# Kernel optimization log

Measured on AMD Instinct MI355X. Metric: run time of the kernel, lower is better.

## Reference

```python
import jax, jax.numpy as jnp
import numpy as np
from jax import lax

V, E, H = 32000, 512, 512
B, T = 16, 128


def setup_inputs() -> dict:
    key = jax.random.key(0)
    ks = jax.random.split(key, 10)
    xs = jax.random.randint(ks[0], (B, T), 0, V)
    xs_len = jax.random.randint(ks[1], (B,), 1, T)
    enc_h = jax.random.normal(ks[2], (1, B, H), dtype=jnp.float32)
    enc_c = jax.random.normal(ks[3], (1, B, H), dtype=jnp.float32)
    emb = jax.random.normal(ks[4], (V, E), dtype=jnp.float32) * 0.02
    emb = emb.at[0].set(0.0)  # padding_idx=0
    s = 1.0 / np.sqrt(H)
    W_ih = jax.random.uniform(ks[5], (4 * H, E), minval=-s, maxval=s, dtype=jnp.float32)
    W_hh = jax.random.uniform(ks[6], (4 * H, H), minval=-s, maxval=s, dtype=jnp.float32)
    b_ih = jax.random.uniform(ks[7], (4 * H,), minval=-s, maxval=s, dtype=jnp.float32)
    b_hh = jax.random.uniform(ks[8], (4 * H,), minval=-s, maxval=s, dtype=jnp.float32)
    W_out = jax.random.normal(ks[9], (V, H), dtype=jnp.float32) * 0.02
    b_out = jnp.zeros((V,), dtype=jnp.float32)
    return {"xs": xs, "xs_len": xs_len, "enc_h": enc_h, "enc_c": enc_c,
            "emb": emb, "W_ih": W_ih, "W_hh": W_hh, "b_ih": b_ih,
            "b_hh": b_hh, "W_out": W_out, "b_out": b_out}


def reference(xs, xs_len, enc_h, enc_c, emb, W_ih, W_hh, b_ih, b_hh, W_out, b_out):
    exs = emb[xs]                         # [B, T, E]
    exs_t = jnp.transpose(exs, (1, 0, 2))  # time-major [T, B, E]

    def step(carry, x):
        h, c = carry
        gates = x @ W_ih.T + b_ih + h @ W_hh.T + b_hh  # [B, 4H]
        i, f, g, o = jnp.split(gates, 4, axis=-1)
        i = jax.nn.sigmoid(i)
        f = jax.nn.sigmoid(f)
        g = jnp.tanh(g)
        o = jax.nn.sigmoid(o)
        c = f * c + i * g
        h = o * jnp.tanh(c)
        return (h, c), h

    _, hs = lax.scan(step, (enc_h[0], enc_c[0]), exs_t)  # hs: [T, B, H]
    cat_hs = hs.reshape(T * B, H)          # torch.cat(hs_list, dim=0)
    logits = cat_hs @ W_out.T + b_out      # [T*B, V]
    return logits
```

## Files before the change

### kernel.cpp

```cpp
#include <hip/hip_runtime.h>
#include <stdint.h>
#include <stddef.h>

#define AS1 __attribute__((address_space(1)))
#define AS3 __attribute__((address_space(3)))

typedef __attribute__((ext_vector_type(4))) float f32x4;
typedef __attribute__((ext_vector_type(8))) short bf16x8;

static __device__ __forceinline__ unsigned short f2b(float x) {
  union { float f; uint32_t u; } c; c.f = x;
  return (unsigned short)((c.u + 0x7FFFu + ((c.u >> 16) & 1u)) >> 16);
}
static __device__ __forceinline__ float fsig(float x) {
  return __builtin_amdgcn_rcpf(1.f + __expf(-x));
}
static __device__ __forceinline__ float ftanh(float x) {
  return 1.f - 2.f * __builtin_amdgcn_rcpf(__expf(2.f * x) + 1.f);
}

#define AGLD(p) __hip_atomic_load((p), __ATOMIC_RELAXED, __HIP_MEMORY_SCOPE_AGENT)
#define AGST(p, v) __hip_atomic_store((p), (v), __ATOMIC_RELAXED, __HIP_MEMORY_SCOPE_AGENT)


__global__ __launch_bounds__(128) void k_cvt_perm(const float* __restrict__ s,
                                                  unsigned short* __restrict__ d) {
  int rp = blockIdx.x;
  int w = rp >> 6, q = (rp >> 4) & 3, j = rp & 15;
  int rs = q * 512 + w * 16 + j;
  float4 v = ((const float4*)(s + (size_t)rs * 512))[threadIdx.x];
  ushort4 o;
  o.x = f2b(v.x); o.y = f2b(v.y); o.z = f2b(v.z); o.w = f2b(v.w);
  ((ushort4*)(d + (size_t)rp * 512))[threadIdx.x] = o;
}

__global__ __launch_bounds__(256) void k_bias_perm(const float* __restrict__ a,
                                                   const float* __restrict__ b,
                                                   float* __restrict__ o) {
  int rp = blockIdx.x * 256 + threadIdx.x;
  if (rp < 2048) {
    int w = rp >> 6, q = (rp >> 4) & 3, j = rp & 15;
    int rs = q * 512 + w * 16 + j;
    o[rp] = a[rs] + b[rs];
  }
}

__global__ __launch_bounds__(128) void k_emb_gather(const int* __restrict__ xs,
                                                    const float* __restrict__ emb,
                                                    unsigned short* __restrict__ out) {
  int m = blockIdx.x;
  int tok = xs[(m & 15) * 128 + (m >> 4)];
  float4 v = ((const float4*)(emb + (size_t)tok * 512))[threadIdx.x];
  ushort4 o;
  o.x = f2b(v.x); o.y = f2b(v.y); o.z = f2b(v.z); o.w = f2b(v.w);
  ((ushort4*)(out + (size_t)m * 512))[threadIdx.x] = o;
}

__global__ __launch_bounds__(256) void k_ench(const float* __restrict__ ench,
                                              unsigned short* __restrict__ hsb) {
  int idx = blockIdx.x * 256 + threadIdx.x;
  int b = idx >> 9, c = idx & 511;
  hsb[(c >> 4) * 256 + b * 16 + (c & 15)] = f2b(ench[b * 512 + c]);
}

__global__ __launch_bounds__(256) void k_gemm_bt(const unsigned short* __restrict__ A,
                                                 const unsigned short* __restrict__ Bt,
                                                 const float* __restrict__ bias,
                                                 float* __restrict__ C,
                                                 int M, int N, int K) {
  __shared__ unsigned short As[128 * 32];
  __shared__ unsigned short Bs[128 * 32];
  const int tiles_n = N >> 7;
  const int tm = blockIdx.x / tiles_n;
  const int tn = blockIdx.x % tiles_n;
  const int m0 = tm << 7, n0 = tn << 7;
  const int tid = threadIdx.x;
  const int wave = tid >> 6, lane = tid & 63;
  const int wr = wave >> 1, wc = wave & 1;
  f32x4 acc[4][4] = {};

  const int lo = wave * 2048 + lane * 16;
  for (int k0 = 0; k0 < K; k0 += 32) {
#pragma unroll
    for (int i = 0; i < 2; ++i) {
      int o = lo + i * 1024;
      int row = o >> 6, kb = o & 63;
      __builtin_amdgcn_global_load_lds(
          (const AS1 uint32_t*)((const char*)A + ((size_t)(m0 + row) * K + k0) * 2 + kb),
          (AS3 uint32_t*)((char*)As + wave * 2048 + i * 1024), 16, 0, 0);
    }
#pragma unroll
    for (int i = 0; i < 2; ++i) {
      int o = lo + i * 1024;
      int row = o >> 6, kb = o & 63;
      __builtin_amdgcn_global_load_lds(
          (const AS1 uint32_t*)((const char*)Bt + ((size_t)(n0 + row) * K + k0) * 2 + kb),
          (AS3 uint32_t*)((char*)Bs + wave * 2048 + i * 1024), 16, 0, 0);
    }
    __syncthreads();
    bf16x8 af[4], bfr[4];
    const int lrow = lane & 15;
    const int kb16 = (lane >> 4) * 16;
#pragma unroll
    for (int i = 0; i < 4; ++i)
      af[i] = *(const bf16x8*)((const char*)As + (wr * 64 + i * 16 + lrow) * 64 + kb16);
#pragma unroll
    for (int j = 0; j < 4; ++j)
      bfr[j] = *(const bf16x8*)((const char*)Bs + (wc * 64 + j * 16 + lrow) * 64 + kb16);
#pragma unroll
    for (int i = 0; i < 4; ++i)
#pragma unroll
      for (int j = 0; j < 4; ++j)
        acc[i][j] = __builtin_amdgcn_mfma_f32_16x16x32_bf16(af[i], bfr[j], acc[i][j], 0, 0, 0);
    __syncthreads();
  }
#pragma unroll
  for (int j = 0; j < 4; ++j) {
    int col = n0 + wc * 64 + j * 16 + (lane & 15);
    float bv = bias[col];
#pragma unroll
    for (int i = 0; i < 4; ++i) {
      int r0 = m0 + wr * 64 + i * 16 + (lane >> 4) * 4;
#pragma unroll
      for (int r = 0; r < 4; ++r)
        C[(size_t)(r0 + r) * N + col] = acc[i][j][r] + bv;
    }
  }
}


__global__ __launch_bounds__(256, 1) void k_fused(
    const float* __restrict__ gp, const unsigned short* __restrict__ wp,
    const float* __restrict__ encc, unsigned short* __restrict__ hsb,
    uint32_t* __restrict__ flags, uint32_t* __restrict__ progress,
    const float* __restrict__ Wout, unsigned short* __restrict__ woutb,
    const float* __restrict__ bout, float* __restrict__ out,
    uint32_t* __restrict__ ticket, uint32_t* __restrict__ cvt_done) {
  __shared__ unsigned short Bs[128 * 32];
  __shared__ int sh_tile;
  __shared__ int sh_rdy;

  const int bid = blockIdx.x;
  const int tid = threadIdx.x;

  const uint64_t K1 = 0x0001000100010001ull;
  const uint64_t K8 = 0x8000800080008000ull;

  if (bid < 32) {
    if (tid >= 64) return;
    const int w = bid;
    const int l = tid;
    const int lr = l & 15;
    const int lk = l >> 4;
    const int col = w * 16 + lr;

    bf16x8 bfr[4][16];
#pragma unroll
    for (int j = 0; j < 4; ++j)
#pragma unroll
      for (int ks = 0; ks < 16; ++ks)
        bfr[j][ks] = *(const bf16x8*)((const char*)wp +
            (size_t)(w * 64 + j * 16 + lr) * 1024 + ks * 64 + lk * 16);

    float cst[4];
#pragma unroll
    for (int r = 0; r < 4; ++r) cst[r] = encc[(lk * 4 + r) * 512 + col];

    const int u64off = (lk >> 1) * 64 + lr * 4 + (lk & 1) * 2;

    float gnx[4][4];
#pragma unroll
    for (int j = 0; j < 4; ++j)
#pragma unroll
      for (int r = 0; r < 4; ++r)
        gnx[j][r] = gp[(size_t)(lk * 4 + r) * 2048 + w * 64 + j * 16 + lr];

    for (int t = 0; t < 128; ++t) {
      f32x4 acc[4];
#pragma unroll
      for (int j = 0; j < 4; ++j)
#pragma unroll
        for (int r = 0; r < 4; ++r) acc[j][r] = gnx[j][r];

      union AF { uint64_t q[2]; bf16x8 v; } af[16];
      const uint64_t* hb = (const uint64_t*)(hsb + (size_t)t * 8192);
      {
        int guard = 0;
        for (;;) {
#pragma unroll
          for (int ks = 0; ks < 16; ++ks) {
            af[ks].q[0] = AGLD(hb + u64off + ks * 128);
            af[ks].q[1] = AGLD(hb + u64off + ks * 128 + 1);
          }
          uint64_t bad = 0;
#pragma unroll
          for (int ks = 0; ks < 16; ++ks) {
            bad |= (~af[ks].q[0] - K1) & af[ks].q[0] & K8;
            bad |= (~af[ks].q[1] - K1) & af[ks].q[1] & K8;
          }
          if (__all(bad == 0)) break;
          if (++guard > (1 << 20)) break;
        }
      }

#pragma unroll
      for (int ks = 0; ks < 16; ++ks) {
#pragma unroll
        for (int j = 0; j < 4; ++j)
          acc[j] = __builtin_amdgcn_mfma_f32_16x16x32_bf16(af[ks].v, bfr[j][ks],
                                                           acc[j], 0, 0, 0);
      }

      uint32_t pk[4];
#pragma unroll
      for (int r = 0; r < 4; ++r) {
        float iv = fsig(acc[0][r]);
        float fv = fsig(acc[1][r]);
        float gv = ftanh(acc[2][r]);
        float ov = fsig(acc[3][r]);
        cst[r] = fv * cst[r] + iv * gv;
        float hv = ov * ftanh(cst[r]);
        uint32_t mine = f2b(hv);
        uint32_t other = (uint32_t)__shfl_xor((int)mine, 1);
        pk[r] = mine | (other << 16);
      }
      uint32_t* hout = (uint32_t*)(hsb + (size_t)(t + 1) * 8192);
      if ((lr & 1) == 0) {
#pragma unroll
        for (int r = 0; r < 4; ++r)
          AGST(hout + w * 128 + (lk * 4 + r) * 8 + (lr >> 1), pk[r]);
      }
      if ((t & 7) == 7 && l == 0)
        AGST(flags + (size_t)(t >> 3) * 32 + w, 1u);

      if (t < 127) {
#pragma unroll
        for (int j = 0; j < 4; ++j)
#pragma unroll
          for (int r = 0; r < 4; ++r)
            gnx[j][r] = gp[(size_t)((t + 1) * 16 + lk * 4 + r) * 2048 +
                           w * 64 + j * 16 + lr];
      }
    }
  } else if (bid == 32) {
    if (tid >= 64) return;
    const int l = tid;
    for (int g = 0; g < 16; ++g) {
      int guard = 0;
      for (;;) {
        uint32_t fl = AGLD(flags + (size_t)g * 32 + (l & 31));
        if (__all(fl != 0u)) break;
        __builtin_amdgcn_s_sleep(4);
        if (++guard > (1 << 18)) break;
      }
      if (l < 8)
        AGST(progress + l * 64, (uint32_t)((g + 1) * 8));
    }
  } else {
    {
      const int gid = bid - 33;
      const int CH = 19052;
      int start = gid * CH;
      int end = start + CH; if (end > 4096000) end = 4096000;
      for (int idx = start + tid; idx < end; idx += 256) {
        float4 v = ((const float4*)Wout)[idx];
        uint32_t lo2 = (uint32_t)f2b(v.x) | ((uint32_t)f2b(v.y) << 16);
        uint32_t hi2 = (uint32_t)f2b(v.z) | ((uint32_t)f2b(v.w) << 16);
        AGST((uint64_t*)woutb + idx, (uint64_t)lo2 | ((uint64_t)hi2 << 32));
      }
      asm volatile("s_waitcnt vmcnt(0)" ::: "memory");
      __syncthreads();
      if (tid == 0) {
        atomicAdd(cvt_done, 1u);
        sh_rdy = 0;
      }
      __syncthreads();
      int guard = 0;
      for (;;) {
        if (tid == 0 && AGLD(cvt_done) >= 215u) sh_rdy = 1;
        __syncthreads();
        if (sh_rdy) break;
        __builtin_amdgcn_s_sleep(16);
        if (++guard > (1 << 18)) break;
        __syncthreads();
      }
    }

    const int wave = tid >> 6, lane = tid & 63;
    const int wr = wave >> 1, wc = wave & 1;
    const int lrow = lane & 15;
    const int ksl = lane >> 4;
    const int lo = wave * 2048 + lane * 16;
    const uint32_t* prog = progress + (bid & 7) * 64;
    const uint64_t* Ab64 = (const uint64_t*)(hsb + 8192);

    for (;;) {
      if (tid == 0) sh_tile = (int)atomicAdd(ticket, 1u);
      __syncthreads();
      const int tk = sh_tile;
      __syncthreads();
      if (tk >= 730) break;
      int m, nb0, ntiles;
      if (tk < 480) {
        m = tk >> 5;
        nb0 = (tk & 31) * 8;
        ntiles = (250 - nb0) < 8 ? (250 - nb0) : 8;
      } else {
        m = 15;
        nb0 = tk - 480;
        ntiles = 1;
      }
      const int m0 = m << 7;
      const uint32_t need = (uint32_t)(m * 8 + 8);

      if (tid == 0) sh_rdy = 0;
      __syncthreads();
      {
        int guard = 0;
        for (;;) {
          if (tid == 0) {
            uint32_t v = AGLD(prog);
            if (v >= need) sh_rdy = 1;
          }
          __syncthreads();
          if (sh_rdy) break;
          __builtin_amdgcn_s_sleep(48);
          if (++guard > (1 << 16)) break;
          __syncthreads();
        }
      }

      {
        int ph = tk & 7;
        for (int s = 0; s < ph; ++s) __builtin_amdgcn_s_sleep(16);
      }

      bf16x8 Areg[16][4];
      {
        int guard = 0;
        for (;;) {
          uint64_t bad = 0;
#pragma unroll
          for (int ks = 0; ks < 16; ++ks)
#pragma unroll
            for (int i = 0; i < 4; ++i) {
              const uint64_t* ap = Ab64 + (size_t)(m * 8 + wr * 4 + i) * 2048 +
                  (2 * ks + (ksl >> 1)) * 64 + lrow * 4 + (ksl & 1) * 2;
              union { uint64_t q[2]; bf16x8 v; } u;
              u.q[0] = AGLD(ap);
              u.q[1] = AGLD(ap + 1);
              bad |= ((~u.q[0] - K1) & u.q[0] & K8) |
                     ((~u.q[1] - K1) & u.q[1] & K8);
              Areg[ks][i] = u.v;
            }
          if (__all(bad == 0)) break;
          __builtin_amdgcn_s_sleep(4);
          if (++guard > (1 << 20)) break;
        }
      }

      for (int jt = 0; jt < ntiles; ++jt) {
        const int n0 = (nb0 + jt) << 7;
        f32x4 acc[4][4] = {};
#pragma unroll
        for (int ks = 0; ks < 16; ++ks) {
#pragma unroll
          for (int i = 0; i < 2; ++i) {
            int o = lo + i * 1024;
            int row = o >> 6, kb = o & 63;
            __builtin_amdgcn_global_load_lds(
                (const AS1 uint32_t*)((const char*)woutb +
                    ((size_t)(n0 + row) * 512 + ks * 32) * 2 + kb),
                (AS3 uint32_t*)((char*)Bs + o), 16, 0, 0);
          }
          __syncthreads();
          bf16x8 bfr[4];
#pragma unroll
          for (int j = 0; j < 4; ++j)
            bfr[j] = *(const bf16x8*)((const char*)Bs +
                (wc * 64 + j * 16 + lrow) * 64 + ksl * 16);
#pragma unroll
          for (int i = 0; i < 4; ++i)
#pragma unroll
            for (int j = 0; j < 4; ++j)
              acc[i][j] = __builtin_amdgcn_mfma_f32_16x16x32_bf16(
                  Areg[ks][i], bfr[j], acc[i][j], 0, 0, 0);
          __syncthreads();
        }
#pragma unroll
        for (int j = 0; j < 4; ++j) {
          int colq = n0 + wc * 64 + j * 16 + (lane & 15);
          float bv = bout[colq];
#pragma unroll
          for (int i = 0; i < 4; ++i) {
            int r0 = m0 + wr * 64 + i * 16 + (lane >> 4) * 4;
#pragma unroll
            for (int r = 0; r < 4; ++r)
              out[(size_t)(r0 + r) * 32000 + colq] = acc[i][j][r] + bv;
          }
        }
      }
    }
  }
}


extern "C" void kernel_launch(void* const* d_in, const int* in_sizes, int n_in,
                              void* d_out, int out_size, void* d_ws, size_t ws_size,
                              hipStream_t stream) {
  (void)in_sizes; (void)n_in; (void)out_size; (void)ws_size;
  const int* xs = (const int*)d_in[0];
  const float* ench = (const float*)d_in[2];
  const float* encc = (const float*)d_in[3];
  const float* emb  = (const float*)d_in[4];
  const float* Wih  = (const float*)d_in[5];
  const float* Whh  = (const float*)d_in[6];
  const float* bih  = (const float*)d_in[7];
  const float* bhh  = (const float*)d_in[8];
  const float* Wout = (const float*)d_in[9];
  const float* bout = (const float*)d_in[10];
  float* out = (float*)d_out;

  char* ws = (char*)d_ws;
  size_t off = 0;
  auto take = [&](size_t bytes) {
    char* p = ws + off;
    off += (bytes + 255) & ~(size_t)255;
    return p;
  };
  float* gates_pre      = (float*)take(2048ull * 2048 * 4);
  unsigned short* hsb   = (unsigned short*)take(129ull * 16 * 512 * 2);
  unsigned short* aemb  = (unsigned short*)take(2048ull * 512 * 2);
  unsigned short* wih_b = (unsigned short*)take(2048ull * 512 * 2);
  unsigned short* wp_b  = (unsigned short*)take(2048ull * 512 * 2);
  unsigned short* wout_b= (unsigned short*)take(32000ull * 512 * 2);
  float* bias1          = (float*)take(2048 * 4);
  uint32_t* flags       = (uint32_t*)take(16ull * 32 * 4);
  uint32_t* progress    = (uint32_t*)take(8 * 256);
  uint32_t* ticket      = (uint32_t*)take(256);
  uint32_t* cvt_done    = (uint32_t*)take(256);

  k_cvt_perm<<<2048, 128, 0, stream>>>(Wih, wih_b);
  k_cvt_perm<<<2048, 128, 0, stream>>>(Whh, wp_b);
  k_emb_gather<<<2048, 128, 0, stream>>>(xs, emb, aemb);
  k_bias_perm<<<8, 256, 0, stream>>>(bih, bhh, bias1);

  k_ench<<<32, 256, 0, stream>>>(ench, hsb);
  hipMemsetAsync(hsb + 16 * 512, 0xFF, 128ull * 16 * 512 * 2, stream);
  hipMemsetAsync(flags, 0, 16ull * 32 * 4, stream);
  hipMemsetAsync(progress, 0, 8 * 256, stream);
  hipMemsetAsync(ticket, 0, 256, stream);
  hipMemsetAsync(cvt_done, 0, 256, stream);

  k_gemm_bt<<<256, 256, 0, stream>>>(aemb, wih_b, bias1, gates_pre, 2048, 2048, 512);

  k_fused<<<248, 256, 0, stream>>>(gates_pre, wp_b, encc, hsb, flags, progress,
                                   Wout, wout_b, bout, out, ticket, cvt_done);
}
```

Before: 425.8 us.

## Fuse input-projection GEMM into persistent kernel, overlapping with recurrence via sentinels

Removes the separate input-gate GEMM launch and has the worker blocks of the persistent kernel compute the gates_pre tiles through a ticket counter. The recurrent blocks poll gates_pre for a 0xFF sentinel, which is set by a memset, before consuming each timestep, so the recurrence can start before the GEMM finishes. Progress flags are also made per-timestep instead of every 8 steps, so the output GEMM can follow the recurrence more closely. The cost is an extra 16MB memset, spin polling on gates_pre, and a wait (waitcnt) before each flag store.

```diff
diff --git a/kernel.cpp b/kernel.cpp
--- a/kernel.cpp
+++ b/kernel.cpp
@@ -63,71 +63,6 @@
   hsb[(c >> 4) * 256 + b * 16 + (c & 15)] = f2b(ench[b * 512 + c]);
 }
 
-__global__ __launch_bounds__(256) void k_gemm_bt(const unsigned short* __restrict__ A,
-                                                 const unsigned short* __restrict__ Bt,
-                                                 const float* __restrict__ bias,
-                                                 float* __restrict__ C,
-                                                 int M, int N, int K) {
-  __shared__ unsigned short As[128 * 32];
-  __shared__ unsigned short Bs[128 * 32];
-  const int tiles_n = N >> 7;
-  const int tm = blockIdx.x / tiles_n;
-  const int tn = blockIdx.x % tiles_n;
-  const int m0 = tm << 7, n0 = tn << 7;
-  const int tid = threadIdx.x;
-  const int wave = tid >> 6, lane = tid & 63;
-  const int wr = wave >> 1, wc = wave & 1;
-  f32x4 acc[4][4] = {};
-
-  const int lo = wave * 2048 + lane * 16;
-  for (int k0 = 0; k0 < K; k0 += 32) {
-#pragma unroll
-    for (int i = 0; i < 2; ++i) {
-      int o = lo + i * 1024;
-      int row = o >> 6, kb = o & 63;
-      __builtin_amdgcn_global_load_lds(
-          (const AS1 uint32_t*)((const char*)A + ((size_t)(m0 + row) * K + k0) * 2 + kb),
-          (AS3 uint32_t*)((char*)As + wave * 2048 + i * 1024), 16, 0, 0);
-    }
-#pragma unroll
-    for (int i = 0; i < 2; ++i) {
-      int o = lo + i * 1024;
-      int row = o >> 6, kb = o & 63;
-      __builtin_amdgcn_global_load_lds(
-          (const AS1 uint32_t*)((const char*)Bt + ((size_t)(n0 + row) * K + k0) * 2 + kb),
-          (AS3 uint32_t*)((char*)Bs + wave * 2048 + i * 1024), 16, 0, 0);
-    }
-    __syncthreads();
-    bf16x8 af[4], bfr[4];
-    const int lrow = lane & 15;
-    const int kb16 = (lane >> 4) * 16;
-#pragma unroll
-    for (int i = 0; i < 4; ++i)
-      af[i] = *(const bf16x8*)((const char*)As + (wr * 64 + i * 16 + lrow) * 64 + kb16);
-#pragma unroll
-    for (int j = 0; j < 4; ++j)
-      bfr[j] = *(const bf16x8*)((const char*)Bs + (wc * 64 + j * 16 + lrow) * 64 + kb16);
-#pragma unroll
-    for (int i = 0; i < 4; ++i)
-#pragma unroll
-      for (int j = 0; j < 4; ++j)
-        acc[i][j] = __builtin_amdgcn_mfma_f32_16x16x32_bf16(af[i], bfr[j], acc[i][j], 0, 0, 0);
-    __syncthreads();
-  }
-#pragma unroll
-  for (int j = 0; j < 4; ++j) {
-    int col = n0 + wc * 64 + j * 16 + (lane & 15);
-    float bv = bias[col];
-#pragma unroll
-    for (int i = 0; i < 4; ++i) {
-      int r0 = m0 + wr * 64 + i * 16 + (lane >> 4) * 4;
-#pragma unroll
-      for (int r = 0; r < 4; ++r)
-        C[(size_t)(r0 + r) * N + col] = acc[i][j][r] + bv;
-    }
-  }
-}
-
 
 __global__ __launch_bounds__(256, 1) void k_fused(
     const float* __restrict__ gp, const unsigned short* __restrict__ wp,
@@ -135,7 +70,11 @@
     uint32_t* __restrict__ flags, uint32_t* __restrict__ progress,
     const float* __restrict__ Wout, unsigned short* __restrict__ woutb,
     const float* __restrict__ bout, float* __restrict__ out,
-    uint32_t* __restrict__ ticket, uint32_t* __restrict__ cvt_done) {
+    const unsigned short* __restrict__ aemb, const unsigned short* __restrict__ wihb,
+    const float* __restrict__ bias1, float* __restrict__ gates_pre,
+    uint32_t* __restrict__ ticket, uint32_t* __restrict__ ticket_g,
+    uint32_t* __restrict__ cvt_done) {
+  __shared__ unsigned short As[128 * 32];
   __shared__ unsigned short Bs[128 * 32];
   __shared__ int sh_tile;
   __shared__ int sh_rdy;
@@ -169,11 +108,35 @@
     const int u64off = (lk >> 1) * 64 + lr * 4 + (lk & 1) * 2;
 
     float gnx[4][4];
-#pragma unroll
-    for (int j = 0; j < 4; ++j)
-#pragma unroll
-      for (int r = 0; r < 4; ++r)
-        gnx[j][r] = gp[(size_t)(lk * 4 + r) * 2048 + w * 64 + j * 16 + lr];
+    const uint32_t* g32 = (const uint32_t*)gp;
+    auto load_gp = [&](int tt) {
+      int guard = 0;
+      for (;;) {
+        uint32_t v[4][4];
+        uint32_t bad = 0;
+#pragma unroll
+        for (int j = 0; j < 4; ++j)
+#pragma unroll
+          for (int r = 0; r < 4; ++r) {
+            v[j][r] = AGLD(g32 + (size_t)(tt * 16 + lk * 4 + r) * 2048 +
+                           w * 64 + j * 16 + lr);
+            bad |= (uint32_t)(v[j][r] == 0xFFFFFFFFu);
+          }
+        if (__all(bad == 0)) {
+#pragma unroll
+          for (int j = 0; j < 4; ++j)
+#pragma unroll
+            for (int r = 0; r < 4; ++r) {
+              union { uint32_t u; float f; } cv; cv.u = v[j][r];
+              gnx[j][r] = cv.f;
+            }
+          return;
+        }
+        __builtin_amdgcn_s_sleep(2);
+        if (++guard > (1 << 20)) return;
+      }
+    };
+    load_gp(0);
 
     for (int t = 0; t < 128; ++t) {
       f32x4 acc[4];
@@ -230,33 +193,91 @@
         for (int r = 0; r < 4; ++r)
           AGST(hout + w * 128 + (lk * 4 + r) * 8 + (lr >> 1), pk[r]);
       }
-      if ((t & 7) == 7 && l == 0)
-        AGST(flags + (size_t)(t >> 3) * 32 + w, 1u);
-
-      if (t < 127) {
-#pragma unroll
-        for (int j = 0; j < 4; ++j)
-#pragma unroll
-          for (int r = 0; r < 4; ++r)
-            gnx[j][r] = gp[(size_t)((t + 1) * 16 + lk * 4 + r) * 2048 +
-                           w * 64 + j * 16 + lr];
-      }
+      asm volatile("s_waitcnt vmcnt(0)" ::: "memory");
+      if (l == 0)
+        AGST(flags + (size_t)t * 32 + w, 1u);
+
+      if (t < 127) load_gp(t + 1);
     }
   } else if (bid == 32) {
     if (tid >= 64) return;
     const int l = tid;
-    for (int g = 0; g < 16; ++g) {
+    for (int t = 0; t < 128; ++t) {
       int guard = 0;
       for (;;) {
-        uint32_t fl = AGLD(flags + (size_t)g * 32 + (l & 31));
+        uint32_t fl = AGLD(flags + (size_t)t * 32 + (l & 31));
         if (__all(fl != 0u)) break;
         __builtin_amdgcn_s_sleep(4);
         if (++guard > (1 << 18)) break;
       }
       if (l < 8)
-        AGST(progress + l * 64, (uint32_t)((g + 1) * 8));
+        AGST(progress + l * 64, (uint32_t)(t + 1));
     }
   } else {
+    const int wave = tid >> 6, lane = tid & 63;
+    const int wr = wave >> 1, wc = wave & 1;
+    const int lrow = lane & 15;
+    const int ksl = lane >> 4;
+    const int lo = wave * 2048 + lane * 16;
+
+    for (;;) {
+      if (tid == 0) sh_tile = (int)atomicAdd(ticket_g, 1u);
+      __syncthreads();
+      const int tkg = sh_tile;
+      __syncthreads();
+      if (tkg >= 256) break;
+      const int gm0 = (tkg >> 4) << 7;
+      const int gn0 = (tkg & 15) << 7;
+      f32x4 acc[4][4] = {};
+      for (int k0 = 0; k0 < 512; k0 += 32) {
+#pragma unroll
+        for (int i2 = 0; i2 < 2; ++i2) {
+          int o = lo + i2 * 1024;
+          int row = o >> 6, kb = o & 63;
+          __builtin_amdgcn_global_load_lds(
+              (const AS1 uint32_t*)((const char*)aemb +
+                  ((size_t)(gm0 + row) * 512 + k0) * 2 + kb),
+              (AS3 uint32_t*)((char*)As + o), 16, 0, 0);
+          __builtin_amdgcn_global_load_lds(
+              (const AS1 uint32_t*)((const char*)wihb +
+                  ((size_t)(gn0 + row) * 512 + k0) * 2 + kb),
+              (AS3 uint32_t*)((char*)Bs + o), 16, 0, 0);
+        }
+        __syncthreads();
+        bf16x8 af2[4], bf2[4];
+        const int kb16 = ksl * 16;
+#pragma unroll
+        for (int i2 = 0; i2 < 4; ++i2)
+          af2[i2] = *(const bf16x8*)((const char*)As +
+              (wr * 64 + i2 * 16 + lrow) * 64 + kb16);
+#pragma unroll
+        for (int j = 0; j < 4; ++j)
+          bf2[j] = *(const bf16x8*)((const char*)Bs +
+              (wc * 64 + j * 16 + lrow) * 64 + kb16);
+#pragma unroll
+        for (int i2 = 0; i2 < 4; ++i2)
+#pragma unroll
+          for (int j = 0; j < 4; ++j)
+            acc[i2][j] = __builtin_amdgcn_mfma_f32_16x16x32_bf16(
+                af2[i2], bf2[j], acc[i2][j], 0, 0, 0);
+        __syncthreads();
+      }
+#pragma unroll
+      for (int j = 0; j < 4; ++j) {
+        int colq = gn0 + wc * 64 + j * 16 + (lane & 15);
+        float bv = bias1[colq];
+#pragma unroll
+        for (int i2 = 0; i2 < 4; ++i2) {
+          int r0 = gm0 + wr * 64 + i2 * 16 + (lane >> 4) * 4;
+#pragma unroll
+          for (int r = 0; r < 4; ++r) {
+            union { float f; uint32_t u; } cv; cv.f = acc[i2][j][r] + bv;
+            AGST((uint32_t*)gates_pre + (size_t)(r0 + r) * 2048 + colq, cv.u);
+          }
+        }
+      }
+    }
+
     {
       const int gid = bid - 33;
       const int CH = 19052;
@@ -286,11 +307,6 @@
       }
     }
 
-    const int wave = tid >> 6, lane = tid & 63;
-    const int wr = wave >> 1, wc = wave & 1;
-    const int lrow = lane & 15;
-    const int ksl = lane >> 4;
-    const int lo = wave * 2048 + lane * 16;
     const uint32_t* prog = progress + (bid & 7) * 64;
     const uint64_t* Ab64 = (const uint64_t*)(hsb + 8192);
 
@@ -435,9 +451,10 @@
   unsigned short* wp_b  = (unsigned short*)take(2048ull * 512 * 2);
   unsigned short* wout_b= (unsigned short*)take(32000ull * 512 * 2);
   float* bias1          = (float*)take(2048 * 4);
-  uint32_t* flags       = (uint32_t*)take(16ull * 32 * 4);
+  uint32_t* flags       = (uint32_t*)take(128ull * 32 * 4);
   uint32_t* progress    = (uint32_t*)take(8 * 256);
   uint32_t* ticket      = (uint32_t*)take(256);
+  uint32_t* ticket_g    = (uint32_t*)take(256);
   uint32_t* cvt_done    = (uint32_t*)take(256);
 
   k_cvt_perm<<<2048, 128, 0, stream>>>(Wih, wih_b);
@@ -447,13 +464,15 @@
 
   k_ench<<<32, 256, 0, stream>>>(ench, hsb);
   hipMemsetAsync(hsb + 16 * 512, 0xFF, 128ull * 16 * 512 * 2, stream);
-  hipMemsetAsync(flags, 0, 16ull * 32 * 4, stream);
+  hipMemsetAsync(gates_pre, 0xFF, 2048ull * 2048 * 4, stream);
+  hipMemsetAsync(flags, 0, 128ull * 32 * 4, stream);
   hipMemsetAsync(progress, 0, 8 * 256, stream);
   hipMemsetAsync(ticket, 0, 256, stream);
+  hipMemsetAsync(ticket_g, 0, 256, stream);
   hipMemsetAsync(cvt_done, 0, 256, stream);
 
-  k_gemm_bt<<<256, 256, 0, stream>>>(aemb, wih_b, bias1, gates_pre, 2048, 2048, 512);
-
   k_fused<<<248, 256, 0, stream>>>(gates_pre, wp_b, encc, hsb, flags, progress,
-                                   Wout, wout_b, bout, out, ticket, cvt_done);
-}
+                                   Wout, wout_b, bout, out,
+                                   aemb, wih_b, bias1, gates_pre,
+                                   ticket, ticket_g, cvt_done);
+}
```

Result: slower. 454.3 us (+6.7%).
